# Optimization experiments

Measured on AMD Instinct MI355X. Metric: run time of the kernel, lower is better.

## Reference

```python
import jax, jax.numpy as jnp
import numpy as np

SR = 44100
SEQ_DUR = 6.0
FBINS = 113
FMIN = 91.6
NSGT_SCALE = 100.0
MIN_WIN = 4


def _mel_frequencies(fmin, fmax, bnds):
    # MelScale from the nsgt package
    hz2mel = lambda f: 1127.01048 * np.log(f / 700.0 + 1.0)
    mel2hz = lambda m: (np.exp(m / 1127.01048) - 1.0) * 700.0
    mmin, mmax = hz2mel(fmin), hz2mel(fmax)
    mbnd = (mmax - mmin) / (bnds - 1)
    return mel2hz(np.arange(bnds) * mbnd + mmin)


def _hannwin(l):
    # fft-centered hann window (peak at index 0), as in nsgt.util.hannwin
    r = np.arange(l, dtype=np.float64) * (2.0 * np.pi / l)
    return 0.5 * (np.cos(r) + 1.0)


def _build_nsgt_params(Ls):
    """Replicates nsgfwin(sliced=False) + calcwinrange + matrixform nsgtf layout.
    Returns G[n_bins, maxLg] (window values, zero where padded) and
    idx[n_bins, maxLg] (gather indices into the length-Ls spectrum)."""
    f = _mel_frequencies(FMIN, SR / 2.0, FBINS)
    nf = SR / 2.0
    lim = int(np.argmax(f > 0))
    if lim != 0:
        f = f[lim:]
    lim = int(np.argmax(f >= nf))
    if lim != 0:
        f = f[:lim]
    lbas = len(f)
    frqs = np.concatenate(((0.0,), f, (nf,)))
    fbas = np.concatenate((frqs, SR - frqs[-2:0:-1]))
    fbas *= float(Ls) / SR
    # bandwidths M[k] (samples)
    M = np.zeros(fbas.shape, dtype=np.int64)
    M[0] = np.round(2 * fbas[1])
    for k in range(1, 2 * lbas + 1):
        M[k] = np.round(fbas[k + 1] - fbas[k - 1])
    M[-1] = np.round(Ls - fbas[-2])
    M = np.clip(M, MIN_WIN, None)
    g = [_hannwin(m) for m in M]
    fbas[lbas] = (fbas[lbas - 1] + fbas[lbas + 1]) / 2
    fbas[lbas + 2] = Ls - fbas[lbas]
    rfbas = np.round(fbas).astype(np.int64)  # window center positions (= timepos)
    # real=True, reducedform=0 -> keep bins 0 .. len(g)//2 (DC..Nyquist)
    n_bins = len(g) // 2 + 1
    maxLg = int(M.max())  # matrixform: every bin padded (in the middle) to max bandwidth
    idx = np.zeros((n_bins, maxLg), dtype=np.int32)
    G = np.zeros((n_bins, maxLg), dtype=np.float32)
    for j in range(n_bins):
        gj = g[j]
        Lg = len(gj)
        tp = int(rfbas[j])
        h = (Lg + 1) // 2  # positive-frequency half
        nh = Lg // 2       # negative-frequency half
        idx[j, :h] = (tp + np.arange(h)) % Ls
        G[j, :h] = gj[:h]
        if nh > 0:
            idx[j, maxLg - nh:] = (tp - nh + np.arange(nh)) % Ls
            G[j, maxLg - nh:] = gj[h:]
    return G, idx


def setup_inputs() -> dict:
    key = jax.random.key(0)
    S, C = 16, 2
    Ls = int(SEQ_DUR * SR)
    x = jax.random.normal(key, (S, C, Ls), dtype=jnp.float32)
    G, idx = _build_nsgt_params(Ls)
    return {"x": x, "G": jnp.asarray(G), "idx": jnp.asarray(idx)}


def reference(x, G, idx):
    # x: (S, C, Ls); G, idx: (n_bins, maxLg)
    S, C, T = x.shape
    ft = jnp.fft.fft(x.reshape(S * C, T))      # (N, Ls) complex64
    c = ft[:, idx] * G                         # (N, n_bins, maxLg): windowed spectrum slices
    coefs = jnp.fft.ifft(c, axis=-1)           # per-bin time frames (matrixform NSGT coeffs)
    coefs = coefs.reshape(S, C, c.shape[1], c.shape[2])
    # torch.view_as_real + * NSGT_SCALE
    return jnp.stack([coefs.real, coefs.imag], axis=-1) * NSGT_SCALE
```

## Files before the change

### kernel.cpp

```cpp
#include <hip/hip_runtime.h>

#define TPB 256
#define TPF 1024
constexpr int LS = 264600;
constexpr int N1 = 525;
constexpr int N2 = 504;
constexpr int ROWS = 32;
constexpr int M_FFT = 16384;
constexpr float TWO_PI_F = 6.28318530717958647692f;
constexpr float PI_F     = 3.14159265358979323846f;

__device__ __forceinline__ int rev7(int x) { return (int)(__brev((unsigned)x) >> 25); }
__device__ __forceinline__ float2 cmul(float2 a, float2 b) {
    return make_float2(a.x * b.x - a.y * b.y, a.x * b.y + a.y * b.x);
}
__device__ __forceinline__ int sidx(int hi, int lo) {
    return (hi << 7) + (lo ^ (hi & 15));
}

__global__ void k0_scan(const float* __restrict__ G, int NL, int* __restrict__ hnh) {
    const int j = blockIdx.x;
    __shared__ int s_first, s_last;
    if (threadIdx.x == 0) { s_first = NL; s_last = -1; }
    __syncthreads();
    const float* Gj = G + (size_t)j * NL;
    for (int m = threadIdx.x; m < NL; m += blockDim.x) {
        if (Gj[m] == 0.0f) {
            atomicMin(&s_first, m);
            atomicMax(&s_last, m);
        }
    }
    __syncthreads();
    if (threadIdx.x == 0) {
        int h  = s_first;
        int nh = (s_last >= 0) ? (NL - 1 - s_last) : 0;
        hnh[2 * j]     = h;
        hnh[2 * j + 1] = nh;
    }
}

__global__ __launch_bounds__(TPB) void k1_dft525(const float* __restrict__ x,
                                                 float2* __restrict__ A) {
    const int n2 = blockIdx.x;
    const int r  = blockIdx.y;
    __shared__ float  xs[N1];
    __shared__ float2 ys[N1];
    __shared__ float2 w25[25];
    __shared__ float2 w21[21];
    const float* xr = x + (size_t)r * LS + n2;
    for (int t = threadIdx.x; t < N1; t += TPB) {
        xs[t] = xr[(size_t)t * N2];
    }
    if (threadIdx.x < 25) {
        float a = -TWO_PI_F * (float)threadIdx.x / 25.0f;
        float s, c; sincosf(a, &s, &c);
        w25[threadIdx.x] = make_float2(c, s);
    } else if (threadIdx.x >= 32 && threadIdx.x < 53) {
        int k = threadIdx.x - 32;
        float a = -TWO_PI_F * (float)k / 21.0f;
        float s, c; sincosf(a, &s, &c);
        w21[k] = make_float2(c, s);
    }
    __syncthreads();
    for (int i = threadIdx.x; i < N1; i += TPB) {
        int alpha = i % 25, b = i / 25;
        float re = 0.f, im = 0.f;
        int iw = 0, it = b;
        #pragma unroll
        for (int a = 0; a < 25; ++a) {
            float  v = xs[it];
            float2 w = w25[iw];
            re = fmaf(v, w.x, re);
            im = fmaf(v, w.y, im);
            it += 21;
            iw += alpha; if (iw >= 25) iw -= 25;
        }
        float ang = -TWO_PI_F * (float)(b * alpha) / (float)N1;
        float s, c; sincosf(ang, &s, &c);
        ys[i] = make_float2(re * c - im * s, re * s + im * c);
    }
    __syncthreads();
    for (int k = threadIdx.x; k < N1; k += TPB) {
        int alpha = k % 25, beta = k / 25;
        float re = 0.f, im = 0.f;
        int iw = 0, iy = alpha;
        #pragma unroll
        for (int b = 0; b < 21; ++b) {
            float2 v = ys[iy];
            float2 w = w21[iw];
            re = fmaf(v.x, w.x, re); re = fmaf(-v.y, w.y, re);
            im = fmaf(v.x, w.y, im); im = fmaf( v.y, w.x, im);
            iy += 25;
            iw += beta; if (iw >= 21) iw -= 21;
        }
        float ang = -TWO_PI_F * (float)(k * n2) / (float)LS;
        float s, c; sincosf(ang, &s, &c);
        A[((size_t)r * N1 + k) * N2 + n2] = make_float2(re * c - im * s, re * s + im * c);
    }
}

__global__ __launch_bounds__(TPB) void k2_dft504(float2* __restrict__ A) {
    const int k1 = blockIdx.x;
    const int r  = blockIdx.y;
    __shared__ float2 as[N2];
    __shared__ float2 ys[N2];
    __shared__ float2 w21[21];
    __shared__ float2 w24[24];
    float2* row = A + ((size_t)r * N1 + k1) * N2;
    for (int t = threadIdx.x; t < N2; t += TPB) as[t] = row[t];
    if (threadIdx.x < 21) {
        float a = -TWO_PI_F * (float)threadIdx.x / 21.0f;
        float s, c; sincosf(a, &s, &c);
        w21[threadIdx.x] = make_float2(c, s);
    } else if (threadIdx.x >= 32 && threadIdx.x < 56) {
        int k = threadIdx.x - 32;
        float a = -TWO_PI_F * (float)k / 24.0f;
        float s, c; sincosf(a, &s, &c);
        w24[k] = make_float2(c, s);
    }
    __syncthreads();
    for (int i = threadIdx.x; i < N2; i += TPB) {
        int alpha = i % 21, b = i / 21;
        float re = 0.f, im = 0.f;
        int iw = 0, it = b;
        #pragma unroll
        for (int a = 0; a < 21; ++a) {
            float2 v = as[it];
            float2 w = w21[iw];
            re = fmaf(v.x, w.x, re); re = fmaf(-v.y, w.y, re);
            im = fmaf(v.x, w.y, im); im = fmaf( v.y, w.x, im);
            it += 24;
            iw += alpha; if (iw >= 21) iw -= 21;
        }
        float ang = -TWO_PI_F * (float)(b * alpha) / (float)N2;
        float s, c; sincosf(ang, &s, &c);
        ys[i] = make_float2(re * c - im * s, re * s + im * c);
    }
    __syncthreads();
    for (int k = threadIdx.x; k < N2; k += TPB) {
        int alpha = k % 21, beta = k / 21;
        float re = 0.f, im = 0.f;
        int iw = 0, iy = alpha;
        #pragma unroll
        for (int b = 0; b < 24; ++b) {
            float2 v = ys[iy];
            float2 w = w24[iw];
            re = fmaf(v.x, w.x, re); re = fmaf(-v.y, w.y, re);
            im = fmaf(v.x, w.y, im); im = fmaf( v.y, w.x, im);
            iy += 21;
            iw += beta; if (iw >= 24) iw -= 24;
        }
        row[k] = make_float2(re, im);
    }
}

__global__ void k_setup(float2* __restrict__ kc, float2* __restrict__ bchirp,
                        float2* __restrict__ twg, int NL) {
    int t = blockIdx.x * blockDim.x + threadIdx.x;
    long long twoNL = 2LL * NL;
    if (t < M_FFT) {
        long long d = 0; bool act = false;
        if (t < NL)              { d = t;        act = true; }
        else if (t > M_FFT - NL) { d = t - M_FFT; act = true; }
        float2 v = make_float2(0.f, 0.f);
        if (act) {
            long long ph = (d * d) % twoNL;
            float th = -PI_F * (float)ph / (float)NL;
            float s, c; sincosf(th, &s, &c);
            v = make_float2(c, s);
        }
        kc[t] = v;
    } else {
        int n = t - M_FFT;
        if (n < NL) {
            long long ph = ((long long)n * n) % twoNL;
            float th = PI_F * (float)ph / (float)NL;
            float s, c; sincosf(th, &s, &c);
            bchirp[n] = make_float2(c, s);
        } else if (n < NL + 64) {
            int q = n - NL;
            float th = -TWO_PI_F * (float)q / 128.0f;
            float s, c; sincosf(th, &s, &c);
            twg[q] = make_float2(c, s);
        }
    }
}

__device__ void fft128_dif(float2 (*ld)[129], const float2* tw, int f, int q) {
    for (int ls = 6; ls >= 0; --ls) {
        int span = 1 << ls;
        for (int b = q; b < 64; b += 16) {
            int j = b & (span - 1);
            int g = b >> ls;
            int u = (g << (ls + 1)) + j;
            int v = u + span;
            float2 A = ld[f][u], B = ld[f][v];
            float2 s = make_float2(A.x + B.x, A.y + B.y);
            float2 d = make_float2(A.x - B.x, A.y - B.y);
            ld[f][u] = s;
            ld[f][v] = cmul(d, tw[j << (6 - ls)]);
        }
        __syncthreads();
    }
}

#define FFT_PROLOG                                                        \
    __shared__ float2 ld[16][129];                                        \
    __shared__ float2 tw[64];                                             \
    if (threadIdx.x < 64) {                                               \
        float th = -TWO_PI_F * (float)threadIdx.x / 128.0f;               \
        float s, c; sincosf(th, &s, &c);                                  \
        tw[threadIdx.x] = make_float2(c, s);                              \
    }

__global__ __launch_bounds__(TPB) void kfft_cols_fwd(float2* __restrict__ P) {
    const int cg = blockIdx.x;
    const size_t vb = (size_t)blockIdx.y * M_FFT;
    FFT_PROLOG
    const int c0 = cg * 16;
    for (int i = threadIdx.x; i < 2048; i += TPB) {
        int cl = i & 15, r = i >> 4;
        ld[cl][r] = P[vb + (c0 + cl) + 128 * r];
    }
    __syncthreads();
    fft128_dif(ld, tw, threadIdx.x >> 4, threadIdx.x & 15);
    for (int i = threadIdx.x; i < 2048; i += TPB) {
        int cl = i & 15, pos = i >> 4;
        int c = c0 + cl;
        int k1 = rev7(pos);
        float th = -TWO_PI_F * (float)(c * k1) / (float)M_FFT;
        float s, co; sincosf(th, &s, &co);
        P[vb + c + 128 * pos] = cmul(ld[cl][pos], make_float2(co, s));
    }
}

__global__ __launch_bounds__(TPB) void kfft_rows_fwd(float2* __restrict__ P) {
    const int rg = blockIdx.x;
    const size_t vb = (size_t)blockIdx.y * M_FFT;
    FFT_PROLOG
    const int R0 = rg * 16;
    for (int i = threadIdx.x; i < 2048; i += TPB) {
        int fl = i >> 7, c = i & 127;
        ld[fl][c] = P[vb + (size_t)(R0 + fl) * 128 + c];
    }
    __syncthreads();
    fft128_dif(ld, tw, threadIdx.x >> 4, threadIdx.x & 15);
    for (int i = threadIdx.x; i < 2048; i += TPB) {
        int fl = i >> 7, pos = i & 127;
        P[vb + (size_t)(R0 + fl) * 128 + pos] = ld[fl][pos];
    }
}

__global__ __launch_bounds__(TPF) void k_fused(const float* __restrict__ Gm,
        const int* __restrict__ idxp, const float2* __restrict__ A,
        const int* __restrict__ hnh, const float2* __restrict__ bchirp,
        const float2* __restrict__ KF, const float2* __restrict__ twg,
        float2* __restrict__ out, int NB, int NL) {
    extern __shared__ float2 mp[];
    const int tid = threadIdx.x;
    const int vg = blockIdx.x;
    const int r = vg / NB, j = vg % NB;
    const int h = hnh[2 * j], nh = hnh[2 * j + 1];
    const int tail0 = NL - nh;
    const float* Gj = Gm + (size_t)j * NL;
    const int*   ij = idxp + (size_t)j * NL;
    const float2* Ar = A + (size_t)r * LS;

    for (int i = tid; i < M_FFT; i += TPF) {
        float2 val = make_float2(0.f, 0.f);
        if (i < h || (i >= tail0 && i < NL)) {
            int k = ij[i];
            float2 f = Ar[(size_t)(k % N1) * N2 + (k / N1)];
            float  g = Gj[i];
            val = cmul(make_float2(f.x * g, f.y * g), bchirp[i]);
        }
        mp[sidx(i >> 7, i & 127)] = val;
    }
    __syncthreads();

    for (int ls = 6; ls >= 0; --ls) {
        const int span = 1 << ls;
        for (int w = tid; w < 8192; w += TPF) {
            const int lo = w & 127, b = w >> 7;
            const int jj = b & (span - 1), g = b >> ls;
            const int u = (g << (ls + 1)) + jj, v = u + span;
            float2 Aa = mp[sidx(u, lo)], Bb = mp[sidx(v, lo)];
            float2 s = make_float2(Aa.x + Bb.x, Aa.y + Bb.y);
            float2 d = make_float2(Aa.x - Bb.x, Aa.y - Bb.y);
            mp[sidx(u, lo)] = s;
            mp[sidx(v, lo)] = cmul(d, twg[jj << (6 - ls)]);
        }
        __syncthreads();
    }
    for (int i = tid; i < M_FFT; i += TPF) {
        const int c = i & 127, pos = i >> 7;
        const int k1 = rev7(pos);
        float th = -TWO_PI_F * (float)(c * k1) / (float)M_FFT;
        float s, co; sincosf(th, &s, &co);
        const int p = sidx(pos, c);
        mp[p] = cmul(mp[p], make_float2(co, s));
    }
    __syncthreads();
    for (int ls = 6; ls >= 0; --ls) {
        const int span = 1 << ls;
        for (int w = tid; w < 8192; w += TPF) {
            const int hi = w & 127, b = w >> 7;
            const int jj = b & (span - 1), g = b >> ls;
            const int u = (g << (ls + 1)) + jj, v = u + span;
            float2 Aa = mp[sidx(hi, u)], Bb = mp[sidx(hi, v)];
            float2 s = make_float2(Aa.x + Bb.x, Aa.y + Bb.y);
            float2 d = make_float2(Aa.x - Bb.x, Aa.y - Bb.y);
            mp[sidx(hi, u)] = s;
            mp[sidx(hi, v)] = cmul(d, twg[jj << (6 - ls)]);
        }
        __syncthreads();
    }
    for (int i = tid; i < M_FFT; i += TPF) {
        const int p = sidx(i >> 7, i & 127);
        mp[p] = cmul(mp[p], KF[i]);
    }
    __syncthreads();
    for (int ls = 0; ls <= 6; ++ls) {
        const int span = 1 << ls;
        for (int w = tid; w < 8192; w += TPF) {
            const int hi = w & 127, b = w >> 7;
            const int jj = b & (span - 1), g = b >> ls;
            const int u = (g << (ls + 1)) + jj, v = u + span;
            float2 wv = twg[jj << (6 - ls)]; wv.y = -wv.y;
            float2 Aa = mp[sidx(hi, u)];
            float2 t  = cmul(mp[sidx(hi, v)], wv);
            mp[sidx(hi, u)] = make_float2(Aa.x + t.x, Aa.y + t.y);
            mp[sidx(hi, v)] = make_float2(Aa.x - t.x, Aa.y - t.y);
        }
        __syncthreads();
    }
    for (int i = tid; i < M_FFT; i += TPF) {
        const int pos = i & 127, R = i >> 7;
        const int k1 = rev7(R);
        float th = TWO_PI_F * (float)(k1 * pos) / (float)M_FFT;
        float s, co; sincosf(th, &s, &co);
        const int p = sidx(R, pos);
        mp[p] = cmul(mp[p], make_float2(co, s));
    }
    __syncthreads();
    for (int ls = 0; ls <= 6; ++ls) {
        const int span = 1 << ls;
        for (int w = tid; w < 8192; w += TPF) {
            const int lo = w & 127, b = w >> 7;
            const int jj = b & (span - 1), g = b >> ls;
            const int u = (g << (ls + 1)) + jj, v = u + span;
            float2 wv = twg[jj << (6 - ls)]; wv.y = -wv.y;
            float2 Aa = mp[sidx(u, lo)];
            float2 t  = cmul(mp[sidx(v, lo)], wv);
            mp[sidx(u, lo)] = make_float2(Aa.x + t.x, Aa.y + t.y);
            mp[sidx(v, lo)] = make_float2(Aa.x - t.x, Aa.y - t.y);
        }
        __syncthreads();
    }
    const float sc = 100.0f / ((float)NL * (float)M_FFT);
    float2* outv = out + (size_t)vg * NL;
    for (int n = tid; n < NL; n += TPF) {
        float2 y = cmul(mp[sidx(n >> 7, n & 127)], bchirp[n]);
        outv[n] = make_float2(y.x * sc, y.y * sc);
    }
}

__global__ __launch_bounds__(TPB) void k3_idft(const float* __restrict__ G,
                                               const int*  __restrict__ idxp,
                                               const float2* __restrict__ FT,
                                               const int*  __restrict__ hnh,
                                               float2* __restrict__ out,
                                               int NB, int NL) {
    extern __shared__ float2 cls[];
    const int j = blockIdx.x;
    const int r = blockIdx.y;
    const int h  = hnh[2 * j];
    const int nh = hnh[2 * j + 1];
    const int Lg = h + nh;
    const float* Gj = G    + (size_t)j * NL;
    const int*   ij = idxp + (size_t)j * NL;

    for (int t = threadIdx.x; t < Lg; t += TPB) {
        int m = (t < h) ? t : (NL - nh + (t - h));
        int k = ij[m];
        float2 f = FT[((size_t)r * N1 + (k % N1)) * N2 + (k / N1)];
        float  g = Gj[m];
        cls[t] = make_float2(f.x * g, f.y * g);
    }
    __syncthreads();

    const float scale = 100.0f / (float)NL;
    const float w0 = TWO_PI_F / (float)NL;
    float2* outr = out + ((size_t)r * NB + j) * NL;

    for (int n_base = 0; n_base < NL; n_base += 4 * TPB) {
        int   n[4];
        float are[4], aim[4], twr[4], twi[4], str[4], sti[4];
        #pragma unroll
        for (int u = 0; u < 4; ++u) {
            n[u] = n_base + u * TPB + (int)threadIdx.x;
            are[u] = 0.f; aim[u] = 0.f;
            float s, c; sincosf(w0 * (float)(n[u] % NL), &s, &c);
            str[u] = c; sti[u] = s;
            twr[u] = 1.f; twi[u] = 0.f;
        }
        for (int t = 0; t < h; ++t) {
            if ((t & 255) == 0) {
                #pragma unroll
                for (int u = 0; u < 4; ++u) {
                    int mm = (int)(((long long)t * (long long)n[u]) % NL);
                    float s, c; sincosf(w0 * (float)mm, &s, &c);
                    twr[u] = c; twi[u] = s;
                }
            }
            float2 cv = cls[t];
            #pragma unroll
            for (int u = 0; u < 4; ++u) {
                are[u] = fmaf(cv.x, twr[u], are[u]);
                are[u] = fmaf(-cv.y, twi[u], are[u]);
                aim[u] = fmaf(cv.x, twi[u], aim[u]);
                aim[u] = fmaf(cv.y, twr[u], aim[u]);
                float nr = twr[u] * str[u] - twi[u] * sti[u];
                float ni = twr[u] * sti[u] + twi[u] * str[u];
                twr[u] = nr; twi[u] = ni;
            }
        }
        const int m0 = NL - nh;
        for (int t = 0; t < nh; ++t) {
            if ((t & 255) == 0) {
                #pragma unroll
                for (int u = 0; u < 4; ++u) {
                    int mm = (int)(((long long)(m0 + t) * (long long)n[u]) % NL);
                    float s, c; sincosf(w0 * (float)mm, &s, &c);
                    twr[u] = c; twi[u] = s;
                }
            }
            float2 cv = cls[h + t];
            #pragma unroll
            for (int u = 0; u < 4; ++u) {
                are[u] = fmaf(cv.x, twr[u], are[u]);
                are[u] = fmaf(-cv.y, twi[u], are[u]);
                aim[u] = fmaf(cv.x, twi[u], aim[u]);
                aim[u] = fmaf(cv.y, twr[u], aim[u]);
                float nr = twr[u] * str[u] - twi[u] * sti[u];
                float ni = twr[u] * sti[u] + twi[u] * str[u];
                twr[u] = nr; twi[u] = ni;
            }
        }
        #pragma unroll
        for (int u = 0; u < 4; ++u) {
            if (n[u] < NL) outr[n[u]] = make_float2(are[u] * scale, aim[u] * scale);
        }
    }
}

static inline size_t align256(size_t x) { return (x + 255) & ~(size_t)255; }

extern "C" void kernel_launch(void* const* d_in, const int* in_sizes, int n_in,
                              void* d_out, int out_size, void* d_ws, size_t ws_size,
                              hipStream_t stream) {
    const float* x   = (const float*)d_in[0];
    const float* Gm  = (const float*)d_in[1];
    const int*   idx = (const int*)d_in[2];
    float2*      out = (float2*)d_out;

    const int p  = in_sizes[1];
    const int NB = (p % 114 == 0) ? 114 : 115;
    const int NL = p / NB;
    const int B  = NB * ROWS;

    size_t hnh_off    = 0;
    size_t bchirp_off = align256(hnh_off + 2048);
    size_t twg_off    = align256(bchirp_off + (size_t)NL * 8);
    size_t kc_off     = align256(twg_off + 64 * 8);
    size_t A_off      = align256(kc_off + (size_t)M_FFT * 8);
    size_t need       = A_off + (size_t)ROWS * LS * 8;

    int*    hnh    = (int*)((char*)d_ws + hnh_off);
    float2* bchirp = (float2*)((char*)d_ws + bchirp_off);
    float2* twg    = (float2*)((char*)d_ws + twg_off);
    float2* kc     = (float2*)((char*)d_ws + kc_off);
    float2* A      = (float2*)((char*)d_ws + A_off);

    k0_scan<<<dim3(NB), TPB, 0, stream>>>(Gm, NL, hnh);
    k1_dft525<<<dim3(N2, ROWS), TPB, 0, stream>>>(x, A);
    k2_dft504<<<dim3(N1, ROWS), TPB, 0, stream>>>(A);

    const bool fused_ok = (2 * NL - 1 <= M_FFT) && (need <= ws_size);
    if (fused_ok) {
        (void)hipFuncSetAttribute((const void*)k_fused,
                                  hipFuncAttributeMaxDynamicSharedMemorySize,
                                  M_FFT * (int)sizeof(float2));
        int setup_blocks = (M_FFT + NL + 64 + TPB - 1) / TPB;
        k_setup<<<dim3(setup_blocks), TPB, 0, stream>>>(kc, bchirp, twg, NL);
        kfft_cols_fwd<<<dim3(8, 1), TPB, 0, stream>>>(kc);
        kfft_rows_fwd<<<dim3(8, 1), TPB, 0, stream>>>(kc);
        k_fused<<<dim3(B), TPF, (size_t)M_FFT * sizeof(float2), stream>>>(
            Gm, idx, A, hnh, bchirp, kc, twg, out, NB, NL);
    } else {
        k3_idft<<<dim3(NB, ROWS), TPB, (size_t)NL * sizeof(float2), stream>>>(
            Gm, idx, A, hnh, out, NB, NL);
    }
}
```

Measured before the change: 1.504 ms.

## Restructure Bluestein FFTs into register radix-4/radix-8 passes with precomputed twiddles

Replaces the radix-2 shared-memory FFT stages in the fused Bluestein kernel with register-held radix-4 pairs and radix-8 butterflies, cutting the number of shared-memory round trips and barriers per 16384-point transform. Per-element sincosf twiddle computation is replaced by a precomputed global twiddle table. The chirp spectrum is now computed by one dedicated kernel into its own buffer. The gather is fused into the first butterfly pass and the last pass into the output scaling. It adds register pressure at 1024 threads, and gather-table twiddle loads that may partly miss cache.

```diff
diff --git a/kernel.cpp b/kernel.cpp
--- a/kernel.cpp
+++ b/kernel.cpp
@@ -14,8 +14,192 @@
 __device__ __forceinline__ float2 cmul(float2 a, float2 b) {
     return make_float2(a.x * b.x - a.y * b.y, a.x * b.y + a.y * b.x);
 }
+__device__ __forceinline__ float2 cmulc(float2 a, float2 w) {
+    return make_float2(a.x * w.x + a.y * w.y, a.y * w.x - a.x * w.y);
+}
+__device__ __forceinline__ float2 cadd(float2 a, float2 b) { return make_float2(a.x + b.x, a.y + b.y); }
+__device__ __forceinline__ float2 csub(float2 a, float2 b) { return make_float2(a.x - b.x, a.y - b.y); }
 __device__ __forceinline__ int sidx(int hi, int lo) {
     return (hi << 7) + (lo ^ (hi & 15));
+}
+template<bool OVER_HI>
+__device__ __forceinline__ int midx(int p, int f) {
+    return OVER_HI ? sidx(p, f) : sidx(f, p);
+}
+
+__device__ __forceinline__ void dif_pair(float2 &v0, float2 &v1, float2 &v2, float2 &v3,
+                                         float2 wA0, float2 wA1, float2 wB) {
+    float2 s0 = cadd(v0, v2), d0 = cmul(csub(v0, v2), wA0);
+    float2 s1 = cadd(v1, v3), d1 = cmul(csub(v1, v3), wA1);
+    v0 = cadd(s0, s1); v1 = cmul(csub(s0, s1), wB);
+    v2 = cadd(d0, d1); v3 = cmul(csub(d0, d1), wB);
+}
+__device__ __forceinline__ void dit_pair(float2 &v0, float2 &v1, float2 &v2, float2 &v3,
+                                         float2 wA, float2 wB0, float2 wB1) {
+    float2 t  = cmulc(v1, wA);
+    float2 a0 = cadd(v0, t), a1 = csub(v0, t);
+    float2 t2 = cmulc(v3, wA);
+    float2 b0 = cadd(v2, t2), b1 = csub(v2, t2);
+    t  = cmulc(b0, wB0); v0 = cadd(a0, t);  v2 = csub(a0, t);
+    t2 = cmulc(b1, wB1); v1 = cadd(a1, t2); v3 = csub(a1, t2);
+}
+
+#define BFLY(u, w, C, S) do {                       \
+    float dx_ = (u).x - (w).x, dy_ = (u).y - (w).y; \
+    (u).x += (w).x; (u).y += (w).y;                 \
+    (w).x = dx_ * (C) - dy_ * (S);                  \
+    (w).y = dx_ * (S) + dy_ * (C);                  \
+} while (0)
+__device__ __forceinline__ void dif8(float2 &b0, float2 &b1, float2 &b2, float2 &b3,
+                                     float2 &b4, float2 &b5, float2 &b6, float2 &b7) {
+    constexpr float r2 = 0.70710678118654752f;
+    BFLY(b0, b4, 1.f, 0.f);
+    BFLY(b1, b5, r2, -r2);
+    BFLY(b2, b6, 0.f, -1.f);
+    BFLY(b3, b7, -r2, -r2);
+    BFLY(b0, b2, 1.f, 0.f);
+    BFLY(b1, b3, 0.f, -1.f);
+    BFLY(b4, b6, 1.f, 0.f);
+    BFLY(b5, b7, 0.f, -1.f);
+    BFLY(b0, b1, 1.f, 0.f);
+    BFLY(b2, b3, 1.f, 0.f);
+    BFLY(b4, b5, 1.f, 0.f);
+    BFLY(b6, b7, 1.f, 0.f);
+}
+#define DITB(u, w, C, S) do {                                        \
+    float2 t_ = make_float2((w).x * (C) - (w).y * (S),               \
+                            (w).x * (S) + (w).y * (C));              \
+    (w) = csub((u), t_); (u) = cadd((u), t_);                        \
+} while (0)
+__device__ __forceinline__ void dit8(float2 &b0, float2 &b1, float2 &b2, float2 &b3,
+                                     float2 &b4, float2 &b5, float2 &b6, float2 &b7) {
+    constexpr float r2 = 0.70710678118654752f;
+    DITB(b0, b1, 1.f, 0.f);
+    DITB(b2, b3, 1.f, 0.f);
+    DITB(b4, b5, 1.f, 0.f);
+    DITB(b6, b7, 1.f, 0.f);
+    DITB(b0, b2, 1.f, 0.f);
+    DITB(b1, b3, 0.f, 1.f);
+    DITB(b4, b6, 1.f, 0.f);
+    DITB(b5, b7, 0.f, 1.f);
+    DITB(b0, b4, 1.f, 0.f);
+    DITB(b1, b5, r2, r2);
+    DITB(b2, b6, 0.f, 1.f);
+    DITB(b3, b7, -r2, r2);
+}
+
+template<bool OVER_HI>
+__device__ __forceinline__ void sweep_pair6_dif(float2* mp, const float2* tws, int tid) {
+    #pragma unroll
+    for (int it = 0; it < 4; ++it) {
+        int qq = tid + (it << 10);
+        int f = qq & 127, j = qq >> 7;
+        float2 v0 = mp[midx<OVER_HI>(j,      f)];
+        float2 v1 = mp[midx<OVER_HI>(j + 32, f)];
+        float2 v2 = mp[midx<OVER_HI>(j + 64, f)];
+        float2 v3 = mp[midx<OVER_HI>(j + 96, f)];
+        dif_pair(v0, v1, v2, v3, tws[j], tws[j + 32], tws[j << 1]);
+        mp[midx<OVER_HI>(j,      f)] = v0;
+        mp[midx<OVER_HI>(j + 32, f)] = v1;
+        mp[midx<OVER_HI>(j + 64, f)] = v2;
+        mp[midx<OVER_HI>(j + 96, f)] = v3;
+    }
+}
+template<bool OVER_HI>
+__device__ __forceinline__ void sweep_pair4_dif(float2* mp, const float2* tws, int tid) {
+    #pragma unroll
+    for (int it = 0; it < 4; ++it) {
+        int qq = tid + (it << 10);
+        int f = qq & 127, b = qq >> 7;
+        int j = b & 7, g = b >> 3, u = (g << 5) + j;
+        float2 v0 = mp[midx<OVER_HI>(u,      f)];
+        float2 v1 = mp[midx<OVER_HI>(u + 8,  f)];
+        float2 v2 = mp[midx<OVER_HI>(u + 16, f)];
+        float2 v3 = mp[midx<OVER_HI>(u + 24, f)];
+        dif_pair(v0, v1, v2, v3, tws[j << 2], tws[(j + 8) << 2], tws[j << 3]);
+        mp[midx<OVER_HI>(u,      f)] = v0;
+        mp[midx<OVER_HI>(u + 8,  f)] = v1;
+        mp[midx<OVER_HI>(u + 16, f)] = v2;
+        mp[midx<OVER_HI>(u + 24, f)] = v3;
+    }
+}
+template<bool OVER_HI>
+__device__ __forceinline__ void sweep_oct_dif(float2* mp, int tid) {
+    #pragma unroll
+    for (int it = 0; it < 2; ++it) {
+        int qq = tid + (it << 10);
+        int f = qq & 127, u = (qq >> 7) << 3;
+        float2 v0 = mp[midx<OVER_HI>(u,     f)];
+        float2 v1 = mp[midx<OVER_HI>(u + 1, f)];
+        float2 v2 = mp[midx<OVER_HI>(u + 2, f)];
+        float2 v3 = mp[midx<OVER_HI>(u + 3, f)];
+        float2 v4 = mp[midx<OVER_HI>(u + 4, f)];
+        float2 v5 = mp[midx<OVER_HI>(u + 5, f)];
+        float2 v6 = mp[midx<OVER_HI>(u + 6, f)];
+        float2 v7 = mp[midx<OVER_HI>(u + 7, f)];
+        dif8(v0, v1, v2, v3, v4, v5, v6, v7);
+        mp[midx<OVER_HI>(u,     f)] = v0;
+        mp[midx<OVER_HI>(u + 1, f)] = v1;
+        mp[midx<OVER_HI>(u + 2, f)] = v2;
+        mp[midx<OVER_HI>(u + 3, f)] = v3;
+        mp[midx<OVER_HI>(u + 4, f)] = v4;
+        mp[midx<OVER_HI>(u + 5, f)] = v5;
+        mp[midx<OVER_HI>(u + 6, f)] = v6;
+        mp[midx<OVER_HI>(u + 7, f)] = v7;
+    }
+}
+template<bool OVER_HI>
+__device__ __forceinline__ void sweep_pair3_dit(float2* mp, const float2* tws, int tid) {
+    #pragma unroll
+    for (int it = 0; it < 4; ++it) {
+        int qq = tid + (it << 10);
+        int f = qq & 127, b = qq >> 7;
+        int j = b & 7, g = b >> 3, u = (g << 5) + j;
+        float2 v0 = mp[midx<OVER_HI>(u,      f)];
+        float2 v1 = mp[midx<OVER_HI>(u + 8,  f)];
+        float2 v2 = mp[midx<OVER_HI>(u + 16, f)];
+        float2 v3 = mp[midx<OVER_HI>(u + 24, f)];
+        dit_pair(v0, v1, v2, v3, tws[j << 3], tws[j << 2], tws[(j + 8) << 2]);
+        mp[midx<OVER_HI>(u,      f)] = v0;
+        mp[midx<OVER_HI>(u + 8,  f)] = v1;
+        mp[midx<OVER_HI>(u + 16, f)] = v2;
+        mp[midx<OVER_HI>(u + 24, f)] = v3;
+    }
+}
+template<bool OVER_HI>
+__device__ __forceinline__ void sweep_pair5_dit(float2* mp, const float2* tws, int tid) {
+    #pragma unroll
+    for (int it = 0; it < 4; ++it) {
+        int qq = tid + (it << 10);
+        int f = qq & 127, j = qq >> 7;
+        float2 v0 = mp[midx<OVER_HI>(j,      f)];
+        float2 v1 = mp[midx<OVER_HI>(j + 32, f)];
+        float2 v2 = mp[midx<OVER_HI>(j + 64, f)];
+        float2 v3 = mp[midx<OVER_HI>(j + 96, f)];
+        dit_pair(v0, v1, v2, v3, tws[j << 1], tws[j], tws[j + 32]);
+        mp[midx<OVER_HI>(j,      f)] = v0;
+        mp[midx<OVER_HI>(j + 32, f)] = v1;
+        mp[midx<OVER_HI>(j + 64, f)] = v2;
+        mp[midx<OVER_HI>(j + 96, f)] = v3;
+    }
+}
+__device__ __forceinline__ void sweep_pair6_dif_mid(float2* mp, const float2* tws,
+                                                    const float2* twM, int tid) {
+    #pragma unroll
+    for (int it = 0; it < 4; ++it) {
+        int qq = tid + (it << 10);
+        int f = qq & 127, j = qq >> 7;
+        int rf = rev7(f);
+        float2 v0 = cmul(mp[sidx(f, j)],      twM[j * rf]);
+        float2 v1 = cmul(mp[sidx(f, j + 32)], twM[(j + 32) * rf]);
+        float2 v2 = cmul(mp[sidx(f, j + 64)], twM[(j + 64) * rf]);
+        float2 v3 = cmul(mp[sidx(f, j + 96)], twM[(j + 96) * rf]);
+        dif_pair(v0, v1, v2, v3, tws[j], tws[j + 32], tws[j << 1]);
+        mp[sidx(f, j)]      = v0;
+        mp[sidx(f, j + 32)] = v1;
+        mp[sidx(f, j + 64)] = v2;
+        mp[sidx(f, j + 96)] = v3;
+    }
 }
 
 __global__ void k0_scan(const float* __restrict__ G, int NL, int* __restrict__ hnh) {
@@ -155,7 +339,7 @@
 }
 
 __global__ void k_setup(float2* __restrict__ kc, float2* __restrict__ bchirp,
-                        float2* __restrict__ twg, int NL) {
+                        float2* __restrict__ twg, float2* __restrict__ twM, int NL) {
     int t = blockIdx.x * blockDim.x + threadIdx.x;
     long long twoNL = 2LL * NL;
     if (t < M_FFT) {
@@ -177,191 +361,163 @@
             float th = PI_F * (float)ph / (float)NL;
             float s, c; sincosf(th, &s, &c);
             bchirp[n] = make_float2(c, s);
-        } else if (n < NL + 64) {
+        } else if (n < NL + 128) {
             int q = n - NL;
             float th = -TWO_PI_F * (float)q / 128.0f;
             float s, c; sincosf(th, &s, &c);
             twg[q] = make_float2(c, s);
-        }
-    }
-}
-
-__device__ void fft128_dif(float2 (*ld)[129], const float2* tw, int f, int q) {
-    for (int ls = 6; ls >= 0; --ls) {
-        int span = 1 << ls;
-        for (int b = q; b < 64; b += 16) {
-            int j = b & (span - 1);
-            int g = b >> ls;
-            int u = (g << (ls + 1)) + j;
-            int v = u + span;
-            float2 A = ld[f][u], B = ld[f][v];
-            float2 s = make_float2(A.x + B.x, A.y + B.y);
-            float2 d = make_float2(A.x - B.x, A.y - B.y);
-            ld[f][u] = s;
-            ld[f][v] = cmul(d, tw[j << (6 - ls)]);
-        }
-        __syncthreads();
-    }
-}
-
-#define FFT_PROLOG                                                        \
-    __shared__ float2 ld[16][129];                                        \
-    __shared__ float2 tw[64];                                             \
-    if (threadIdx.x < 64) {                                               \
-        float th = -TWO_PI_F * (float)threadIdx.x / 128.0f;               \
-        float s, c; sincosf(th, &s, &c);                                  \
-        tw[threadIdx.x] = make_float2(c, s);                              \
-    }
-
-__global__ __launch_bounds__(TPB) void kfft_cols_fwd(float2* __restrict__ P) {
-    const int cg = blockIdx.x;
-    const size_t vb = (size_t)blockIdx.y * M_FFT;
-    FFT_PROLOG
-    const int c0 = cg * 16;
-    for (int i = threadIdx.x; i < 2048; i += TPB) {
-        int cl = i & 15, r = i >> 4;
-        ld[cl][r] = P[vb + (c0 + cl) + 128 * r];
-    }
-    __syncthreads();
-    fft128_dif(ld, tw, threadIdx.x >> 4, threadIdx.x & 15);
-    for (int i = threadIdx.x; i < 2048; i += TPB) {
-        int cl = i & 15, pos = i >> 4;
-        int c = c0 + cl;
-        int k1 = rev7(pos);
-        float th = -TWO_PI_F * (float)(c * k1) / (float)M_FFT;
-        float s, co; sincosf(th, &s, &co);
-        P[vb + c + 128 * pos] = cmul(ld[cl][pos], make_float2(co, s));
-    }
-}
-
-__global__ __launch_bounds__(TPB) void kfft_rows_fwd(float2* __restrict__ P) {
-    const int rg = blockIdx.x;
-    const size_t vb = (size_t)blockIdx.y * M_FFT;
-    FFT_PROLOG
-    const int R0 = rg * 16;
-    for (int i = threadIdx.x; i < 2048; i += TPB) {
-        int fl = i >> 7, c = i & 127;
-        ld[fl][c] = P[vb + (size_t)(R0 + fl) * 128 + c];
-    }
-    __syncthreads();
-    fft128_dif(ld, tw, threadIdx.x >> 4, threadIdx.x & 15);
-    for (int i = threadIdx.x; i < 2048; i += TPB) {
-        int fl = i >> 7, pos = i & 127;
-        P[vb + (size_t)(R0 + fl) * 128 + pos] = ld[fl][pos];
-    }
-}
+        } else if (n < NL + 128 + M_FFT) {
+            int q = n - NL - 128;
+            float th = -TWO_PI_F * (float)q / (float)M_FFT;
+            float s, c; sincosf(th, &s, &c);
+            twM[q] = make_float2(c, s);
+        }
+    }
+}
+
+__global__ __launch_bounds__(TPF) void k_kf(const float2* __restrict__ kc,
+        const float2* __restrict__ twg, const float2* __restrict__ twM,
+        float2* __restrict__ KF) {
+    extern __shared__ float2 mp[];
+    __shared__ float2 tws[64];
+    const int tid = threadIdx.x;
+    if (tid < 64) tws[tid] = twg[tid];
+    for (int i = tid; i < M_FFT; i += TPF)
+        mp[sidx(i >> 7, i & 127)] = kc[i];
+    __syncthreads();
+    sweep_pair6_dif<true>(mp, tws, tid);  __syncthreads();
+    sweep_pair4_dif<true>(mp, tws, tid);  __syncthreads();
+    sweep_oct_dif<true>(mp, tid);         __syncthreads();
+    sweep_pair6_dif_mid(mp, tws, twM, tid); __syncthreads();
+    sweep_pair4_dif<false>(mp, tws, tid); __syncthreads();
+    sweep_oct_dif<false>(mp, tid);        __syncthreads();
+    for (int i = tid; i < M_FFT; i += TPF)
+        KF[i] = mp[sidx(i >> 7, i & 127)];
+}
+
+#define GATH(var, I) do {                                                     \
+    (var) = make_float2(0.f, 0.f);                                            \
+    const int i_ = (I);                                                       \
+    if (i_ < h || (i_ >= tail0 && i_ < NL)) {                                 \
+        int k_ = ij[i_];                                                      \
+        float2 f_ = Ar[(size_t)(k_ % N1) * N2 + (k_ / N1)];                   \
+        float  g_ = Gj[i_];                                                   \
+        (var) = cmul(make_float2(f_.x * g_, f_.y * g_), bchirp[i_]);          \
+    }                                                                         \
+} while (0)
 
 __global__ __launch_bounds__(TPF) void k_fused(const float* __restrict__ Gm,
         const int* __restrict__ idxp, const float2* __restrict__ A,
         const int* __restrict__ hnh, const float2* __restrict__ bchirp,
         const float2* __restrict__ KF, const float2* __restrict__ twg,
+        const float2* __restrict__ twM,
         float2* __restrict__ out, int NB, int NL) {
     extern __shared__ float2 mp[];
+    __shared__ float2 tws[64];
     const int tid = threadIdx.x;
+    if (tid < 64) tws[tid] = twg[tid];
     const int vg = blockIdx.x;
-    const int r = vg / NB, j = vg % NB;
-    const int h = hnh[2 * j], nh = hnh[2 * j + 1];
+    const int rr_ = vg / NB, jb = vg % NB;
+    const int h = hnh[2 * jb], nh = hnh[2 * jb + 1];
     const int tail0 = NL - nh;
-    const float* Gj = Gm + (size_t)j * NL;
-    const int*   ij = idxp + (size_t)j * NL;
-    const float2* Ar = A + (size_t)r * LS;
-
-    for (int i = tid; i < M_FFT; i += TPF) {
-        float2 val = make_float2(0.f, 0.f);
-        if (i < h || (i >= tail0 && i < NL)) {
-            int k = ij[i];
-            float2 f = Ar[(size_t)(k % N1) * N2 + (k / N1)];
-            float  g = Gj[i];
-            val = cmul(make_float2(f.x * g, f.y * g), bchirp[i]);
-        }
-        mp[sidx(i >> 7, i & 127)] = val;
-    }
-    __syncthreads();
-
-    for (int ls = 6; ls >= 0; --ls) {
-        const int span = 1 << ls;
-        for (int w = tid; w < 8192; w += TPF) {
-            const int lo = w & 127, b = w >> 7;
-            const int jj = b & (span - 1), g = b >> ls;
-            const int u = (g << (ls + 1)) + jj, v = u + span;
-            float2 Aa = mp[sidx(u, lo)], Bb = mp[sidx(v, lo)];
-            float2 s = make_float2(Aa.x + Bb.x, Aa.y + Bb.y);
-            float2 d = make_float2(Aa.x - Bb.x, Aa.y - Bb.y);
-            mp[sidx(u, lo)] = s;
-            mp[sidx(v, lo)] = cmul(d, twg[jj << (6 - ls)]);
-        }
-        __syncthreads();
-    }
-    for (int i = tid; i < M_FFT; i += TPF) {
-        const int c = i & 127, pos = i >> 7;
-        const int k1 = rev7(pos);
-        float th = -TWO_PI_F * (float)(c * k1) / (float)M_FFT;
-        float s, co; sincosf(th, &s, &co);
-        const int p = sidx(pos, c);
-        mp[p] = cmul(mp[p], make_float2(co, s));
-    }
-    __syncthreads();
-    for (int ls = 6; ls >= 0; --ls) {
-        const int span = 1 << ls;
-        for (int w = tid; w < 8192; w += TPF) {
-            const int hi = w & 127, b = w >> 7;
-            const int jj = b & (span - 1), g = b >> ls;
-            const int u = (g << (ls + 1)) + jj, v = u + span;
-            float2 Aa = mp[sidx(hi, u)], Bb = mp[sidx(hi, v)];
-            float2 s = make_float2(Aa.x + Bb.x, Aa.y + Bb.y);
-            float2 d = make_float2(Aa.x - Bb.x, Aa.y - Bb.y);
-            mp[sidx(hi, u)] = s;
-            mp[sidx(hi, v)] = cmul(d, twg[jj << (6 - ls)]);
-        }
-        __syncthreads();
-    }
-    for (int i = tid; i < M_FFT; i += TPF) {
-        const int p = sidx(i >> 7, i & 127);
-        mp[p] = cmul(mp[p], KF[i]);
-    }
-    __syncthreads();
-    for (int ls = 0; ls <= 6; ++ls) {
-        const int span = 1 << ls;
-        for (int w = tid; w < 8192; w += TPF) {
-            const int hi = w & 127, b = w >> 7;
-            const int jj = b & (span - 1), g = b >> ls;
-            const int u = (g << (ls + 1)) + jj, v = u + span;
-            float2 wv = twg[jj << (6 - ls)]; wv.y = -wv.y;
-            float2 Aa = mp[sidx(hi, u)];
-            float2 t  = cmul(mp[sidx(hi, v)], wv);
-            mp[sidx(hi, u)] = make_float2(Aa.x + t.x, Aa.y + t.y);
-            mp[sidx(hi, v)] = make_float2(Aa.x - t.x, Aa.y - t.y);
-        }
-        __syncthreads();
-    }
-    for (int i = tid; i < M_FFT; i += TPF) {
-        const int pos = i & 127, R = i >> 7;
-        const int k1 = rev7(R);
-        float th = TWO_PI_F * (float)(k1 * pos) / (float)M_FFT;
-        float s, co; sincosf(th, &s, &co);
-        const int p = sidx(R, pos);
-        mp[p] = cmul(mp[p], make_float2(co, s));
-    }
-    __syncthreads();
-    for (int ls = 0; ls <= 6; ++ls) {
-        const int span = 1 << ls;
-        for (int w = tid; w < 8192; w += TPF) {
-            const int lo = w & 127, b = w >> 7;
-            const int jj = b & (span - 1), g = b >> ls;
-            const int u = (g << (ls + 1)) + jj, v = u + span;
-            float2 wv = twg[jj << (6 - ls)]; wv.y = -wv.y;
-            float2 Aa = mp[sidx(u, lo)];
-            float2 t  = cmul(mp[sidx(v, lo)], wv);
-            mp[sidx(u, lo)] = make_float2(Aa.x + t.x, Aa.y + t.y);
-            mp[sidx(v, lo)] = make_float2(Aa.x - t.x, Aa.y - t.y);
-        }
-        __syncthreads();
-    }
+    const float* Gj = Gm + (size_t)jb * NL;
+    const int*   ij = idxp + (size_t)jb * NL;
+    const float2* Ar = A + (size_t)rr_ * LS;
+    __syncthreads();
+
+    #pragma unroll
+    for (int it = 0; it < 4; ++it) {
+        int qq = tid + (it << 10);
+        int f = qq & 127, j = qq >> 7;
+        float2 v0, v1, v2, v3;
+        GATH(v0, (j     ) * 128 + f);
+        GATH(v1, (j + 32) * 128 + f);
+        GATH(v2, (j + 64) * 128 + f);
+        GATH(v3, (j + 96) * 128 + f);
+        dif_pair(v0, v1, v2, v3, tws[j], tws[j + 32], tws[j << 1]);
+        mp[sidx(j,      f)] = v0;
+        mp[sidx(j + 32, f)] = v1;
+        mp[sidx(j + 64, f)] = v2;
+        mp[sidx(j + 96, f)] = v3;
+    }
+    __syncthreads();
+    sweep_pair4_dif<true>(mp, tws, tid);  __syncthreads();
+    sweep_oct_dif<true>(mp, tid);         __syncthreads();
+    sweep_pair6_dif_mid(mp, tws, twM, tid); __syncthreads();
+    sweep_pair4_dif<false>(mp, tws, tid); __syncthreads();
+    sweep_oct_dif<false>(mp, tid);        __syncthreads();
+
+    #pragma unroll
+    for (int it = 0; it < 2; ++it) {
+        int qq = tid + (it << 10);
+        int f = qq & 127, u = (qq >> 7) << 3;
+        const float2* KFr = KF + (size_t)f * 128 + u;
+        float2 v0 = cmul(mp[sidx(f, u)],     KFr[0]);
+        float2 v1 = cmul(mp[sidx(f, u + 1)], KFr[1]);
+        float2 v2 = cmul(mp[sidx(f, u + 2)], KFr[2]);
+        float2 v3 = cmul(mp[sidx(f, u + 3)], KFr[3]);
+        float2 v4 = cmul(mp[sidx(f, u + 4)], KFr[4]);
+        float2 v5 = cmul(mp[sidx(f, u + 5)], KFr[5]);
+        float2 v6 = cmul(mp[sidx(f, u + 6)], KFr[6]);
+        float2 v7 = cmul(mp[sidx(f, u + 7)], KFr[7]);
+        dit8(v0, v1, v2, v3, v4, v5, v6, v7);
+        mp[sidx(f, u)]     = v0;
+        mp[sidx(f, u + 1)] = v1;
+        mp[sidx(f, u + 2)] = v2;
+        mp[sidx(f, u + 3)] = v3;
+        mp[sidx(f, u + 4)] = v4;
+        mp[sidx(f, u + 5)] = v5;
+        mp[sidx(f, u + 6)] = v6;
+        mp[sidx(f, u + 7)] = v7;
+    }
+    __syncthreads();
+    sweep_pair3_dit<false>(mp, tws, tid); __syncthreads();
+    sweep_pair5_dit<false>(mp, tws, tid); __syncthreads();
+
+    #pragma unroll
+    for (int it = 0; it < 2; ++it) {
+        int qq = tid + (it << 10);
+        int f = qq & 127, u = (qq >> 7) << 3;
+        float2 v0 = cmulc(mp[sidx(u,     f)], twM[rev7(u)     * f]);
+        float2 v1 = cmulc(mp[sidx(u + 1, f)], twM[rev7(u + 1) * f]);
+        float2 v2 = cmulc(mp[sidx(u + 2, f)], twM[rev7(u + 2) * f]);
+        float2 v3 = cmulc(mp[sidx(u + 3, f)], twM[rev7(u + 3) * f]);
+        float2 v4 = cmulc(mp[sidx(u + 4, f)], twM[rev7(u + 4) * f]);
+        float2 v5 = cmulc(mp[sidx(u + 5, f)], twM[rev7(u + 5) * f]);
+        float2 v6 = cmulc(mp[sidx(u + 6, f)], twM[rev7(u + 6) * f]);
+        float2 v7 = cmulc(mp[sidx(u + 7, f)], twM[rev7(u + 7) * f]);
+        dit8(v0, v1, v2, v3, v4, v5, v6, v7);
+        mp[sidx(u,     f)] = v0;
+        mp[sidx(u + 1, f)] = v1;
+        mp[sidx(u + 2, f)] = v2;
+        mp[sidx(u + 3, f)] = v3;
+        mp[sidx(u + 4, f)] = v4;
+        mp[sidx(u + 5, f)] = v5;
+        mp[sidx(u + 6, f)] = v6;
+        mp[sidx(u + 7, f)] = v7;
+    }
+    __syncthreads();
+    sweep_pair3_dit<true>(mp, tws, tid); __syncthreads();
+
     const float sc = 100.0f / ((float)NL * (float)M_FFT);
     float2* outv = out + (size_t)vg * NL;
-    for (int n = tid; n < NL; n += TPF) {
-        float2 y = cmul(mp[sidx(n >> 7, n & 127)], bchirp[n]);
-        outv[n] = make_float2(y.x * sc, y.y * sc);
+    #pragma unroll
+    for (int it = 0; it < 4; ++it) {
+        int qq = tid + (it << 10);
+        int f = qq & 127, j = qq >> 7;
+        float2 v0 = mp[sidx(j,      f)];
+        float2 v1 = mp[sidx(j + 32, f)];
+        float2 v2 = mp[sidx(j + 64, f)];
+        float2 v3 = mp[sidx(j + 96, f)];
+        dit_pair(v0, v1, v2, v3, tws[j << 1], tws[j], tws[j + 32]);
+        int n0 = (j)      * 128 + f;
+        int n1 = (j + 32) * 128 + f;
+        int n2_ = (j + 64) * 128 + f;
+        int n3 = (j + 96) * 128 + f;
+        if (n0 < NL) { float2 y = cmul(v0, bchirp[n0]); outv[n0] = make_float2(y.x * sc, y.y * sc); }
+        if (n1 < NL) { float2 y = cmul(v1, bchirp[n1]); outv[n1] = make_float2(y.x * sc, y.y * sc); }
+        if (n2_ < NL) { float2 y = cmul(v2, bchirp[n2_]); outv[n2_] = make_float2(y.x * sc, y.y * sc); }
+        if (n3 < NL) { float2 y = cmul(v3, bchirp[n3]); outv[n3] = make_float2(y.x * sc, y.y * sc); }
     }
 }
 
@@ -472,14 +628,18 @@
     size_t hnh_off    = 0;
     size_t bchirp_off = align256(hnh_off + 2048);
     size_t twg_off    = align256(bchirp_off + (size_t)NL * 8);
-    size_t kc_off     = align256(twg_off + 64 * 8);
-    size_t A_off      = align256(kc_off + (size_t)M_FFT * 8);
+    size_t twM_off    = align256(twg_off + 128 * 8);
+    size_t kc_off     = align256(twM_off + (size_t)M_FFT * 8);
+    size_t kf_off     = align256(kc_off + (size_t)M_FFT * 8);
+    size_t A_off      = align256(kf_off + (size_t)M_FFT * 8);
     size_t need       = A_off + (size_t)ROWS * LS * 8;
 
     int*    hnh    = (int*)((char*)d_ws + hnh_off);
     float2* bchirp = (float2*)((char*)d_ws + bchirp_off);
     float2* twg    = (float2*)((char*)d_ws + twg_off);
+    float2* twM    = (float2*)((char*)d_ws + twM_off);
     float2* kc     = (float2*)((char*)d_ws + kc_off);
+    float2* KF     = (float2*)((char*)d_ws + kf_off);
     float2* A      = (float2*)((char*)d_ws + A_off);
 
     k0_scan<<<dim3(NB), TPB, 0, stream>>>(Gm, NL, hnh);
@@ -491,12 +651,14 @@
         (void)hipFuncSetAttribute((const void*)k_fused,
                                   hipFuncAttributeMaxDynamicSharedMemorySize,
                                   M_FFT * (int)sizeof(float2));
-        int setup_blocks = (M_FFT + NL + 64 + TPB - 1) / TPB;
-        k_setup<<<dim3(setup_blocks), TPB, 0, stream>>>(kc, bchirp, twg, NL);
-        kfft_cols_fwd<<<dim3(8, 1), TPB, 0, stream>>>(kc);
-        kfft_rows_fwd<<<dim3(8, 1), TPB, 0, stream>>>(kc);
+        (void)hipFuncSetAttribute((const void*)k_kf,
+                                  hipFuncAttributeMaxDynamicSharedMemorySize,
+                                  M_FFT * (int)sizeof(float2));
+        int setup_blocks = (2 * M_FFT + NL + 128 + TPB - 1) / TPB;
+        k_setup<<<dim3(setup_blocks), TPB, 0, stream>>>(kc, bchirp, twg, twM, NL);
+        k_kf<<<dim3(1), TPF, (size_t)M_FFT * sizeof(float2), stream>>>(kc, twg, twM, KF);
         k_fused<<<dim3(B), TPF, (size_t)M_FFT * sizeof(float2), stream>>>(
-            Gm, idx, A, hnh, bchirp, kc, twg, out, NB, NL);
+            Gm, idx, A, hnh, bchirp, KF, twg, twM, out, NB, NL);
     } else {
         k3_idft<<<dim3(NB, ROWS), TPB, (size_t)NL * sizeof(float2), stream>>>(
             Gm, idx, A, hnh, out, NB, NL);
```

After: 1.315 ms. 12.6% less time.
